# Kernel optimization log

Hardware: AMD Instinct MI355X
Metric: run time of the kernel (lower is better)

The kernel has to match this reference:

```python
import jax, jax.numpy as jnp
import numpy as np

N = 10000          # nodes
E = 160000         # edges (avg degree 16)
F = 240            # invariant features_dim
H_INV, D_INV = 4, 60    # invariant heads / head dim
H_EV, D_EV = 3, 80      # equivariant heads (= len(degrees)) / head dim
RBF = 32
DEGREES = [1, 2, 3]
REPEATS = np.array([2 * l + 1 for l in DEGREES])   # [3,5,7]
EV_DIM = int(REPEATS.sum())                        # 15
OFFS = np.concatenate([[0], np.cumsum(REPEATS)])   # [0,3,8,15]


def _kaiming_uniform(key, shape, fan_in):
    # torch kaiming_uniform_ with a=sqrt(5): bound = 1/sqrt(fan_in)
    b = 1.0 / np.sqrt(fan_in)
    return jax.random.uniform(key, shape, minval=-b, maxval=b, dtype=jnp.float32)


def setup_inputs() -> dict:
    key = jax.random.key(0)
    ks = jax.random.split(key, 16)
    return {
        "inv_features": jax.random.normal(ks[0], (N, F), dtype=jnp.float32),
        "ev_features": jax.random.normal(ks[1], (N, EV_DIM), dtype=jnp.float32),
        "rbf": jax.random.uniform(ks[2], (E, RBF), dtype=jnp.float32),
        "sh_vectors": jax.random.normal(ks[3], (E, EV_DIM), dtype=jnp.float32),
        "cutoffs": jax.random.uniform(ks[4], (E, 1), dtype=jnp.float32),
        "W_q_inv": _kaiming_uniform(ks[5], (H_INV, D_INV, D_INV), D_INV),
        "W_k_inv": _kaiming_uniform(ks[6], (H_INV, D_INV, D_INV), D_INV),
        "W_v_inv": _kaiming_uniform(ks[7], (H_INV, D_INV, D_INV), D_INV),
        "W_q_ev": _kaiming_uniform(ks[8], (H_EV, D_EV, D_EV), D_EV),
        "W_k_ev": _kaiming_uniform(ks[9], (H_EV, D_EV, D_EV), D_EV),
        "W_filt_inv": _kaiming_uniform(ks[10], (RBF + len(DEGREES), F), RBF + len(DEGREES)),
        "b_filt_inv": jnp.zeros((F,), dtype=jnp.float32),
        "W_filt_ev": _kaiming_uniform(ks[11], (RBF + len(DEGREES), F), RBF + len(DEGREES)),
        "b_filt_ev": jnp.zeros((F,), dtype=jnp.float32),
        "senders": jax.random.randint(ks[12], (E,), 0, N, dtype=jnp.int32),
        "receivers": jax.random.randint(ks[13], (E,), 0, N, dtype=jnp.int32),
    }


def reference(inv_features, ev_features, rbf, sh_vectors, cutoffs,
              W_q_inv, W_k_inv, W_v_inv, W_q_ev, W_k_ev,
              W_filt_inv, b_filt_inv, W_filt_ev, b_filt_ev,
              senders, receivers):
    n = inv_features.shape[0]
    # edge-wise equivariant differences [E, 15]
    ev_diff = ev_features[senders] - ev_features[receivers]
    # per-degree SO3 invariants: sum over m components of each degree -> [E, 3]
    invs = jnp.stack([(ev_diff[:, OFFS[i]:OFFS[i + 1]] ** 2).sum(-1)
                      for i in range(len(DEGREES))], axis=-1)
    f_in = jnp.concatenate([rbf, invs], axis=-1)           # [E, RBF+3]
    fw_inv = (f_in @ W_filt_inv + b_filt_inv).reshape(-1, H_INV, D_INV)
    fw_ev = (f_in @ W_filt_ev + b_filt_ev).reshape(-1, H_EV, D_EV)

    xi = inv_features.reshape(-1, H_INV, D_INV)
    xe = inv_features.reshape(-1, H_EV, D_EV)
    q_inv = jnp.einsum('hij,nhi->nhj', W_q_inv, xi)[receivers]
    k_inv = jnp.einsum('hij,nhi->nhj', W_k_inv, xi)[senders]
    v_inv = jnp.einsum('hij,nhi->nhj', W_v_inv, xi)[senders]
    q_ev = jnp.einsum('hij,nhi->nhj', W_q_ev, xe)[receivers]
    k_ev = jnp.einsum('hij,nhi->nhj', W_k_ev, xe)[senders]

    alpha_inv = (q_inv * (k_inv * fw_inv)).sum(-1, keepdims=True) / np.sqrt(D_INV)  # [E,H,1]
    alpha_ev = (q_ev * (k_ev * fw_ev)).sum(-1) / np.sqrt(D_EV)                      # [E,3]

    scaled_inv = cutoffs[:, None] * alpha_inv * v_inv       # [E,H,D]
    d_inv = jax.ops.segment_sum(scaled_inv, receivers, num_segments=n).reshape(n, -1)

    alpha_ev_r = jnp.repeat(alpha_ev, REPEATS, axis=-1, total_repeat_length=EV_DIM)  # [E,15]
    scaled_ev = cutoffs * alpha_ev_r * sh_vectors
    d_ev = jax.ops.segment_sum(scaled_ev, receivers, num_segments=n)
    return d_inv, d_ev
```

## Files before the change

### kernel.cpp

```cpp
#include <hip/hip_runtime.h>

#define PNPB 32

__global__ __launch_bounds__(512) void proj_kernel(
    const float* __restrict__ x,
    const float* __restrict__ Wq, const float* __restrict__ Wk,
    const float* __restrict__ Wv,
    const float* __restrict__ Wqe, const float* __restrict__ Wke,
    float* __restrict__ q_inv, float* __restrict__ k_inv,
    float* __restrict__ v_inv,
    float* __restrict__ q_ev, float* __restrict__ k_ev, int N)
{
    __shared__ float xs[PNPB * 240];
    const int base_node = blockIdx.x * PNPB;
    for (int idx = threadIdx.x; idx < PNPB * 240; idx += 512) {
        int g = base_node * 240 + idx;
        xs[idx] = (g < N * 240) ? x[g] : 0.f;
    }
    __syncthreads();

    const int slot = threadIdx.x & 63;
    const int wg   = threadIdx.x >> 6;
    if (slot >= 60) return;

    const int hi  = slot / 15;
    const int jdi = slot * 4 - hi * 60;
    const int he  = slot / 20;
    const int jde = slot * 4 - he * 80;
    const int nl0 = wg * 4;

    float4 aq[4], ak[4], av[4], aqe[4], ake[4];
    #pragma unroll
    for (int n = 0; n < 4; ++n) {
        aq[n] = make_float4(0.f,0.f,0.f,0.f); ak[n] = aq[n]; av[n] = aq[n];
        aqe[n] = aq[n]; ake[n] = aq[n];
    }
    {
        const float* wq = Wq + hi * 3600 + jdi;
        const float* wk = Wk + hi * 3600 + jdi;
        const float* wv = Wv + hi * 3600 + jdi;
        const float* xb = &xs[nl0 * 240 + hi * 60];
        #pragma unroll 2
        for (int i = 0; i < 60; ++i) {
            float xv0 = xb[i], xv1 = xb[240 + i], xv2 = xb[480 + i], xv3 = xb[720 + i];
            float4 w;
            w = *(const float4*)&wq[i * 60];
            aq[0].x += xv0*w.x; aq[0].y += xv0*w.y; aq[0].z += xv0*w.z; aq[0].w += xv0*w.w;
            aq[1].x += xv1*w.x; aq[1].y += xv1*w.y; aq[1].z += xv1*w.z; aq[1].w += xv1*w.w;
            aq[2].x += xv2*w.x; aq[2].y += xv2*w.y; aq[2].z += xv2*w.z; aq[2].w += xv2*w.w;
            aq[3].x += xv3*w.x; aq[3].y += xv3*w.y; aq[3].z += xv3*w.z; aq[3].w += xv3*w.w;
            w = *(const float4*)&wk[i * 60];
            ak[0].x += xv0*w.x; ak[0].y += xv0*w.y; ak[0].z += xv0*w.z; ak[0].w += xv0*w.w;
            ak[1].x += xv1*w.x; ak[1].y += xv1*w.y; ak[1].z += xv1*w.z; ak[1].w += xv1*w.w;
            ak[2].x += xv2*w.x; ak[2].y += xv2*w.y; ak[2].z += xv2*w.z; ak[2].w += xv2*w.w;
            ak[3].x += xv3*w.x; ak[3].y += xv3*w.y; ak[3].z += xv3*w.z; ak[3].w += xv3*w.w;
            w = *(const float4*)&wv[i * 60];
            av[0].x += xv0*w.x; av[0].y += xv0*w.y; av[0].z += xv0*w.z; av[0].w += xv0*w.w;
            av[1].x += xv1*w.x; av[1].y += xv1*w.y; av[1].z += xv1*w.z; av[1].w += xv1*w.w;
            av[2].x += xv2*w.x; av[2].y += xv2*w.y; av[2].z += xv2*w.z; av[2].w += xv2*w.w;
            av[3].x += xv3*w.x; av[3].y += xv3*w.y; av[3].z += xv3*w.z; av[3].w += xv3*w.w;
        }
    }
    {
        const float* wq = Wqe + he * 6400 + jde;
        const float* wk = Wke + he * 6400 + jde;
        const float* xb = &xs[nl0 * 240 + he * 80];
        #pragma unroll 2
        for (int i = 0; i < 80; ++i) {
            float xv0 = xb[i], xv1 = xb[240 + i], xv2 = xb[480 + i], xv3 = xb[720 + i];
            float4 w;
            w = *(const float4*)&wq[i * 80];
            aqe[0].x += xv0*w.x; aqe[0].y += xv0*w.y; aqe[0].z += xv0*w.z; aqe[0].w += xv0*w.w;
            aqe[1].x += xv1*w.x; aqe[1].y += xv1*w.y; aqe[1].z += xv1*w.z; aqe[1].w += xv1*w.w;
            aqe[2].x += xv2*w.x; aqe[2].y += xv2*w.y; aqe[2].z += xv2*w.z; aqe[2].w += xv2*w.w;
            aqe[3].x += xv3*w.x; aqe[3].y += xv3*w.y; aqe[3].z += xv3*w.z; aqe[3].w += xv3*w.w;
            w = *(const float4*)&wk[i * 80];
            ake[0].x += xv0*w.x; ake[0].y += xv0*w.y; ake[0].z += xv0*w.z; ake[0].w += xv0*w.w;
            ake[1].x += xv1*w.x; ake[1].y += xv1*w.y; ake[1].z += xv1*w.z; ake[1].w += xv1*w.w;
            ake[2].x += xv2*w.x; ake[2].y += xv2*w.y; ake[2].z += xv2*w.z; ake[2].w += xv2*w.w;
            ake[3].x += xv3*w.x; ake[3].y += xv3*w.y; ake[3].z += xv3*w.z; ake[3].w += xv3*w.w;
        }
    }
    #pragma unroll
    for (int n = 0; n < 4; ++n) {
        const int node = base_node + nl0 + n;
        if (node >= N) break;
        const int ob = node * 240 + slot * 4;
        *(float4*)&q_inv[ob] = aq[n];
        *(float4*)&k_inv[ob] = ak[n];
        *(float4*)&v_inv[ob] = av[n];
        *(float4*)&q_ev[ob]  = aqe[n];
        *(float4*)&k_ev[ob]  = ake[n];
    }
}

__global__ __launch_bounds__(256) void hist_kernel(
    const int* __restrict__ rcv, int* __restrict__ counts, int E)
{
    int e = blockIdx.x * 256 + threadIdx.x;
    if (e < E) atomicAdd(&counts[rcv[e]], 1);
}

__global__ __launch_bounds__(1024) void scan_kernel(
    const int* __restrict__ counts, int* __restrict__ rowstart,
    int* __restrict__ cursor, int N)
{
    __shared__ int wsum[16];
    __shared__ int carry_s;
    if (threadIdx.x == 0) carry_s = 0;
    __syncthreads();
    const int lane = threadIdx.x & 63;
    const int w    = threadIdx.x >> 6;
    for (int base = 0; base < N; base += 1024) {
        const int i = base + threadIdx.x;
        int v = (i < N) ? counts[i] : 0;
        int x = v;
        #pragma unroll
        for (int off = 1; off < 64; off <<= 1) {
            int t = __shfl_up(x, off);
            if (lane >= off) x += t;
        }
        if (lane == 63) wsum[w] = x;
        __syncthreads();
        if (w == 0) {
            int s = (lane < 16) ? wsum[lane] : 0;
            #pragma unroll
            for (int off = 1; off < 16; off <<= 1) {
                int t = __shfl_up(s, off);
                if (lane >= off) s += t;
            }
            if (lane < 16) wsum[lane] = s;
        }
        __syncthreads();
        const int woff = (w == 0) ? 0 : wsum[w - 1];
        const int ex = carry_s + woff + x - v;
        if (i < N) { rowstart[i] = ex; cursor[i] = ex; }
        __syncthreads();
        if (threadIdx.x == 1023) carry_s += wsum[15];
    }
    __syncthreads();
    if (threadIdx.x == 0) rowstart[N] = carry_s;
}

__global__ __launch_bounds__(256) void scatter_kernel(
    const int* __restrict__ rcv, int* __restrict__ cursor,
    int* __restrict__ csr, int E)
{
    int e = blockIdx.x * 256 + threadIdx.x;
    if (e < E) {
        int pos = atomicAdd(&cursor[rcv[e]], 1);
        csr[pos] = e;
    }
}

__global__ __launch_bounds__(256) void inv3_kernel(
    const float* __restrict__ ev_f, const int* __restrict__ snd,
    const int* __restrict__ rcv, float* __restrict__ inv3, int E)
{
    int e = blockIdx.x * 256 + threadIdx.x;
    if (e >= E) return;
    const float* es = ev_f + (size_t)snd[e] * 15;
    const float* er = ev_f + (size_t)rcv[e] * 15;
    float i0 = 0.f, i1 = 0.f, i2 = 0.f;
    #pragma unroll
    for (int q = 0; q < 3; ++q)  { float d = es[q] - er[q]; i0 = fmaf(d, d, i0); }
    #pragma unroll
    for (int q = 3; q < 8; ++q)  { float d = es[q] - er[q]; i1 = fmaf(d, d, i1); }
    #pragma unroll
    for (int q = 8; q < 15; ++q) { float d = es[q] - er[q]; i2 = fmaf(d, d, i2); }
    *(float4*)(inv3 + (size_t)e * 4) = make_float4(i0, i1, i2, 0.f);
}

__global__ __launch_bounds__(256, 1) void alpha_inv_kernel(
    const float* __restrict__ rbf, const float* __restrict__ inv3,
    const float* __restrict__ cut,
    const float* __restrict__ Wfi, const float* __restrict__ bfi,
    const int* __restrict__ snd, const int* __restrict__ rcv,
    const int* __restrict__ csr,
    const float* __restrict__ q_inv, const float* __restrict__ k_inv,
    float* __restrict__ alpha, int E)
{
    __shared__ float fs[4][64 * 36];
    __shared__ int   ss[4][64], sr[4][64];

    const int lane = threadIdx.x & 63;
    const int wid  = threadIdx.x >> 6;
    const int h = lane >> 4;
    const int m = lane & 15;
    const bool act = (m < 15);
    const int j0 = h * 60 + (act ? m * 4 : 0);

    float4 w[35];
    #pragma unroll
    for (int k = 0; k < 35; ++k)
        w[k] = *(const float4*)(Wfi + k * 240 + j0);
    const float4 b4 = *(const float4*)(bfi + j0);
    const float s60 = 0.12909944487358056f;

    const int tbase = (blockIdx.x * 4 + wid) * 64;
    {
        int i = tbase + lane;
        if (i >= E) i = E - 1;
        const int e = csr[i];
        float* frow = &fs[wid][lane * 36];
        const float4* rb = (const float4*)(rbf + (size_t)e * 32);
        #pragma unroll
        for (int k4 = 0; k4 < 8; ++k4)
            *(float4*)&frow[k4 * 4] = rb[k4];
        const float4 v3 = *(const float4*)(inv3 + (size_t)e * 4);
        frow[32] = v3.x; frow[33] = v3.y; frow[34] = v3.z;
        frow[35] = cut[e];
        ss[wid][lane] = snd[e];
        sr[wid][lane] = rcv[e];
    }
    __syncthreads();

    #pragma unroll 2
    for (int t = 0; t < 64; ++t) {
        const int gi = tbase + t;
        if (gi >= E) break;
        const int s = ss[wid][t];
        const int r = sr[wid][t];
        const float* frow = &fs[wid][t * 36];

        float4 fw = b4;
        #pragma unroll
        for (int k4 = 0; k4 < 8; ++k4) {
            const float4 f4 = *(const float4*)&frow[k4 * 4];
            const float4 w0 = w[k4*4+0], w1 = w[k4*4+1], w2 = w[k4*4+2], w3 = w[k4*4+3];
            fw.x = fmaf(f4.x, w0.x, fw.x); fw.y = fmaf(f4.x, w0.y, fw.y);
            fw.z = fmaf(f4.x, w0.z, fw.z); fw.w = fmaf(f4.x, w0.w, fw.w);
            fw.x = fmaf(f4.y, w1.x, fw.x); fw.y = fmaf(f4.y, w1.y, fw.y);
            fw.z = fmaf(f4.y, w1.z, fw.z); fw.w = fmaf(f4.y, w1.w, fw.w);
            fw.x = fmaf(f4.z, w2.x, fw.x); fw.y = fmaf(f4.z, w2.y, fw.y);
            fw.z = fmaf(f4.z, w2.z, fw.z); fw.w = fmaf(f4.z, w2.w, fw.w);
            fw.x = fmaf(f4.w, w3.x, fw.x); fw.y = fmaf(f4.w, w3.y, fw.y);
            fw.z = fmaf(f4.w, w3.z, fw.z); fw.w = fmaf(f4.w, w3.w, fw.w);
        }
        {
            const float fa = frow[32], fb = frow[33], fc = frow[34];
            const float4 wa = w[32], wb = w[33], wc = w[34];
            fw.x = fmaf(fa, wa.x, fw.x); fw.y = fmaf(fa, wa.y, fw.y);
            fw.z = fmaf(fa, wa.z, fw.z); fw.w = fmaf(fa, wa.w, fw.w);
            fw.x = fmaf(fb, wb.x, fw.x); fw.y = fmaf(fb, wb.y, fw.y);
            fw.z = fmaf(fb, wb.z, fw.z); fw.w = fmaf(fb, wb.w, fw.w);
            fw.x = fmaf(fc, wc.x, fw.x); fw.y = fmaf(fc, wc.y, fw.y);
            fw.z = fmaf(fc, wc.z, fw.z); fw.w = fmaf(fc, wc.w, fw.w);
        }
        const float cc = frow[35];

        const float4 q  = *(const float4*)(q_inv + (size_t)r * 240 + j0);
        const float4 kk = *(const float4*)(k_inv + (size_t)s * 240 + j0);
        float d = act ? (q.x*kk.x*fw.x + q.y*kk.y*fw.y
                       + q.z*kk.z*fw.z + q.w*kk.w*fw.w) : 0.f;
        #pragma unroll
        for (int off = 1; off < 16; off <<= 1) d += __shfl_xor(d, off, 16);
        if (m == 0)    alpha[(size_t)gi * 8 + h] = d * s60 * cc;
        if (lane == 0) alpha[(size_t)gi * 8 + 7] = __int_as_float(s);
    }
}

__global__ __launch_bounds__(256, 1) void alpha_ev_kernel(
    const float* __restrict__ rbf, const float* __restrict__ inv3,
    const float* __restrict__ cut,
    const float* __restrict__ Wfe, const float* __restrict__ bfe,
    const int* __restrict__ snd, const int* __restrict__ rcv,
    const int* __restrict__ csr,
    const float* __restrict__ q_ev, const float* __restrict__ k_ev,
    float* __restrict__ alpha, int E)
{
    __shared__ float fs[4][64 * 36];
    __shared__ int   ss[4][64], sr[4][64];

    const int lane = threadIdx.x & 63;
    const int wid  = threadIdx.x >> 6;
    const bool act = (lane < 60);
    const int h = act ? (lane / 20) : 0;
    const int m = act ? (lane % 20) : 0;
    const int j0 = 80 * h + 4 * m;

    float4 w[35];
    #pragma unroll
    for (int k = 0; k < 35; ++k)
        w[k] = *(const float4*)(Wfe + k * 240 + j0);
    const float4 b4 = *(const float4*)(bfe + j0);
    const float s80 = 0.11180339887498948f;

    const int tbase = (blockIdx.x * 4 + wid) * 64;
    {
        int i = tbase + lane;
        if (i >= E) i = E - 1;
        const int e = csr[i];
        float* frow = &fs[wid][lane * 36];
        const float4* rb = (const float4*)(rbf + (size_t)e * 32);
        #pragma unroll
        for (int k4 = 0; k4 < 8; ++k4)
            *(float4*)&frow[k4 * 4] = rb[k4];
        const float4 v3 = *(const float4*)(inv3 + (size_t)e * 4);
        frow[32] = v3.x; frow[33] = v3.y; frow[34] = v3.z;
        frow[35] = cut[e];
        ss[wid][lane] = snd[e];
        sr[wid][lane] = rcv[e];
    }
    __syncthreads();

    #pragma unroll 2
    for (int t = 0; t < 64; ++t) {
        const int gi = tbase + t;
        if (gi >= E) break;
        const int s = ss[wid][t];
        const int r = sr[wid][t];
        const float* frow = &fs[wid][t * 36];

        float4 fw = b4;
        #pragma unroll
        for (int k4 = 0; k4 < 8; ++k4) {
            const float4 f4 = *(const float4*)&frow[k4 * 4];
            const float4 w0 = w[k4*4+0], w1 = w[k4*4+1], w2 = w[k4*4+2], w3 = w[k4*4+3];
            fw.x = fmaf(f4.x, w0.x, fw.x); fw.y = fmaf(f4.x, w0.y, fw.y);
            fw.z = fmaf(f4.x, w0.z, fw.z); fw.w = fmaf(f4.x, w0.w, fw.w);
            fw.x = fmaf(f4.y, w1.x, fw.x); fw.y = fmaf(f4.y, w1.y, fw.y);
            fw.z = fmaf(f4.y, w1.z, fw.z); fw.w = fmaf(f4.y, w1.w, fw.w);
            fw.x = fmaf(f4.z, w2.x, fw.x); fw.y = fmaf(f4.z, w2.y, fw.y);
            fw.z = fmaf(f4.z, w2.z, fw.z); fw.w = fmaf(f4.z, w2.w, fw.w);
            fw.x = fmaf(f4.w, w3.x, fw.x); fw.y = fmaf(f4.w, w3.y, fw.y);
            fw.z = fmaf(f4.w, w3.z, fw.z); fw.w = fmaf(f4.w, w3.w, fw.w);
        }
        {
            const float fa = frow[32], fb = frow[33], fc = frow[34];
            const float4 wa = w[32], wb = w[33], wc = w[34];
            fw.x = fmaf(fa, wa.x, fw.x); fw.y = fmaf(fa, wa.y, fw.y);
            fw.z = fmaf(fa, wa.z, fw.z); fw.w = fmaf(fa, wa.w, fw.w);
            fw.x = fmaf(fb, wb.x, fw.x); fw.y = fmaf(fb, wb.y, fw.y);
            fw.z = fmaf(fb, wb.z, fw.z); fw.w = fmaf(fb, wb.w, fw.w);
            fw.x = fmaf(fc, wc.x, fw.x); fw.y = fmaf(fc, wc.y, fw.y);
            fw.z = fmaf(fc, wc.z, fw.z); fw.w = fmaf(fc, wc.w, fw.w);
        }
        const float cc = frow[35];

        const float4 q  = *(const float4*)(q_ev + (size_t)r * 240 + j0);
        const float4 kk = *(const float4*)(k_ev + (size_t)s * 240 + j0);
        float d = act ? (q.x*kk.x*fw.x + q.y*kk.y*fw.y
                       + q.z*kk.z*fw.z + q.w*kk.w*fw.w) : 0.f;

        float tt;
        tt = __shfl(d, (lane + 10) & 63); if (m < 10) d += tt;
        tt = __shfl(d, (lane + 5) & 63);  if (m < 5)  d += tt;
        const int gb = h * 20;
        const float t1 = __shfl(d, gb + 1);
        const float t2 = __shfl(d, gb + 2);
        const float t3 = __shfl(d, gb + 3);
        const float t4 = __shfl(d, gb + 4);
        if (act && m == 0)
            alpha[(size_t)gi * 8 + 4 + h] = (d + t1 + t2 + t3 + t4) * s80 * cc;
    }
}

__global__ __launch_bounds__(256) void gather_kernel(
    const int* __restrict__ rowstart, const int* __restrict__ csr,
    const float* __restrict__ alpha,
    const float* __restrict__ v_inv, const float* __restrict__ sh,
    float* __restrict__ dinv, float* __restrict__ dev)
{
    const int r = blockIdx.x;
    const int c = threadIdx.x;
    const int beg = rowstart[r], end = rowstart[r + 1];

    __shared__ float sal[64][8];
    __shared__ int   sed[64];

    float acc = 0.f;
    for (int chunk = beg; chunk < end; chunk += 64) {
        const int len = min(64, end - chunk);
        __syncthreads();
        if (c < len) {
            const float4* ap = (const float4*)(alpha + (size_t)(chunk + c) * 8);
            const float4 a0 = ap[0], a1 = ap[1];
            *(float4*)&sal[c][0] = a0;
            *(float4*)&sal[c][4] = a1;
            sed[c] = csr[chunk + c];
        }
        __syncthreads();
        if (c < 240) {
            const int h = c / 60;
            #pragma unroll 4
            for (int i = 0; i < len; ++i) {
                const int s = __float_as_int(sal[i][7]);
                acc += sal[i][h] * v_inv[(size_t)s * 240 + c];
            }
        } else if (c < 255) {
            const int i0 = c - 240;
            const int h = (i0 < 3) ? 4 : ((i0 < 8) ? 5 : 6);
            for (int i = 0; i < len; ++i)
                acc += sal[i][h] * sh[(size_t)sed[i] * 15 + i0];
        }
    }
    if (c < 240) dinv[(size_t)r * 240 + c] = acc;
    else if (c < 255) dev[(size_t)r * 15 + (c - 240)] = acc;
}

extern "C" void kernel_launch(void* const* d_in, const int* in_sizes, int n_in,
                              void* d_out, int out_size, void* d_ws, size_t ws_size,
                              hipStream_t stream) {
    const float* inv_f = (const float*)d_in[0];
    const float* ev_f  = (const float*)d_in[1];
    const float* rbf   = (const float*)d_in[2];
    const float* sh    = (const float*)d_in[3];
    const float* cut   = (const float*)d_in[4];
    const float* Wq    = (const float*)d_in[5];
    const float* Wk    = (const float*)d_in[6];
    const float* Wv    = (const float*)d_in[7];
    const float* Wqe   = (const float*)d_in[8];
    const float* Wke   = (const float*)d_in[9];
    const float* Wfi   = (const float*)d_in[10];
    const float* bfi   = (const float*)d_in[11];
    const float* Wfe   = (const float*)d_in[12];
    const float* bfe   = (const float*)d_in[13];
    const int*   snd   = (const int*)d_in[14];
    const int*   rcv   = (const int*)d_in[15];

    const int N = in_sizes[0] / 240;
    const int E = in_sizes[14];

    float* out  = (float*)d_out;
    float* dinv = out;
    float* dev  = out + (size_t)N * 240;

    float* ws = (float*)d_ws;
    const size_t Nf = (size_t)N * 240;
    float* q_inv = ws + 0 * Nf;
    float* k_inv = ws + 1 * Nf;
    float* v_inv = ws + 2 * Nf;
    float* q_ev  = ws + 3 * Nf;
    float* k_ev  = ws + 4 * Nf;
    float* alpha = ws + 5 * Nf;
    float* inv3  = alpha + (size_t)E * 8;
    int*   ibase    = (int*)(inv3 + (size_t)E * 4);
    int*   counts   = ibase;
    int*   rowstart = ibase + N;
    int*   cursor   = ibase + 2 * N + 1;
    int*   csr      = ibase + 3 * N + 1;

    hipMemsetAsync(counts, 0, (size_t)N * sizeof(int), stream);

    const int eb = (E + 255) / 256;
    hist_kernel<<<eb, 256, 0, stream>>>(rcv, counts, E);
    scan_kernel<<<1, 1024, 0, stream>>>(counts, rowstart, cursor, N);
    scatter_kernel<<<eb, 256, 0, stream>>>(rcv, cursor, csr, E);

    proj_kernel<<<(N + PNPB - 1) / PNPB, 512, 0, stream>>>(
        inv_f, Wq, Wk, Wv, Wqe, Wke, q_inv, k_inv, v_inv, q_ev, k_ev, N);

    inv3_kernel<<<eb, 256, 0, stream>>>(ev_f, snd, rcv, inv3, E);

    const int ab = (E + 255) / 256;
    alpha_inv_kernel<<<ab, 256, 0, stream>>>(
        rbf, inv3, cut, Wfi, bfi, snd, rcv, csr, q_inv, k_inv, alpha, E);
    alpha_ev_kernel<<<ab, 256, 0, stream>>>(
        rbf, inv3, cut, Wfe, bfe, snd, rcv, csr, q_ev, k_ev, alpha, E);

    gather_kernel<<<N, 256, 0, stream>>>(
        rowstart, csr, alpha, v_inv, sh, dinv, dev);
}
```

Before: 386.5 us.

## Merge inv/ev alpha kernels into one 2D-grid launch with smaller tiles

The two per-edge attention-score kernels become one kernel, with blockIdx.y choosing the invariant or equivariant branch. The per-wave edge tile shrinks from 64 to 32, which doubles the block count and reduces shared memory per block. Launch bounds rise from 1 to 4 blocks per SM, aiming for more concurrent waves to hide the gather latency on q/k rows. The cost is that the 35 weight float4s per lane are loaded twice as often, and register pressure must now fit the higher occupancy target.

```diff
diff --git a/kernel.cpp b/kernel.cpp
--- a/kernel.cpp
+++ b/kernel.cpp
@@ -1,6 +1,7 @@
 #include <hip/hip_runtime.h>
 
 #define PNPB 32
+#define TILE 32
 
 __global__ __launch_bounds__(512) void proj_kernel(
     const float* __restrict__ x,
@@ -171,34 +172,49 @@
     *(float4*)(inv3 + (size_t)e * 4) = make_float4(i0, i1, i2, 0.f);
 }
 
-__global__ __launch_bounds__(256, 1) void alpha_inv_kernel(
+__global__ __launch_bounds__(256, 4) void alpha_fused_kernel(
     const float* __restrict__ rbf, const float* __restrict__ inv3,
     const float* __restrict__ cut,
     const float* __restrict__ Wfi, const float* __restrict__ bfi,
+    const float* __restrict__ Wfe, const float* __restrict__ bfe,
     const int* __restrict__ snd, const int* __restrict__ rcv,
     const int* __restrict__ csr,
     const float* __restrict__ q_inv, const float* __restrict__ k_inv,
+    const float* __restrict__ q_ev,  const float* __restrict__ k_ev,
     float* __restrict__ alpha, int E)
 {
-    __shared__ float fs[4][64 * 36];
-    __shared__ int   ss[4][64], sr[4][64];
+    __shared__ float fs[4][TILE * 36];
+    __shared__ int   ss[4][TILE], sr[4][TILE];
 
     const int lane = threadIdx.x & 63;
     const int wid  = threadIdx.x >> 6;
-    const int h = lane >> 4;
-    const int m = lane & 15;
-    const bool act = (m < 15);
-    const int j0 = h * 60 + (act ? m * 4 : 0);
+    const int part = blockIdx.y;
+
+    int h, m, j0; bool act;
+    if (part == 0) {
+        h = lane >> 4; m = lane & 15; act = (m < 15);
+        j0 = h * 60 + (act ? m * 4 : 0);
+    } else {
+        act = (lane < 60);
+        h = act ? (lane / 20) : 0;
+        m = act ? (lane % 20) : 0;
+        j0 = 80 * h + 4 * m;
+    }
+
+    const float* Wf = part ? Wfe : Wfi;
+    const float* bf = part ? bfe : bfi;
+    const float* qbase = part ? q_ev : q_inv;
+    const float* kbase = part ? k_ev : k_inv;
+    const float scale = part ? 0.11180339887498948f : 0.12909944487358056f;
 
     float4 w[35];
     #pragma unroll
     for (int k = 0; k < 35; ++k)
-        w[k] = *(const float4*)(Wfi + k * 240 + j0);
-    const float4 b4 = *(const float4*)(bfi + j0);
-    const float s60 = 0.12909944487358056f;
-
-    const int tbase = (blockIdx.x * 4 + wid) * 64;
-    {
+        w[k] = *(const float4*)(Wf + k * 240 + j0);
+    const float4 b4 = *(const float4*)(bf + j0);
+
+    const int tbase = (blockIdx.x * 4 + wid) * TILE;
+    if (lane < TILE) {
         int i = tbase + lane;
         if (i >= E) i = E - 1;
         const int e = csr[i];
@@ -216,7 +232,7 @@
     __syncthreads();
 
     #pragma unroll 2
-    for (int t = 0; t < 64; ++t) {
+    for (int t = 0; t < TILE; ++t) {
         const int gi = tbase + t;
         if (gi >= E) break;
         const int s = ss[wid][t];
@@ -249,110 +265,28 @@
         }
         const float cc = frow[35];
 
-        const float4 q  = *(const float4*)(q_inv + (size_t)r * 240 + j0);
-        const float4 kk = *(const float4*)(k_inv + (size_t)s * 240 + j0);
+        const float4 q  = *(const float4*)(qbase + (size_t)r * 240 + j0);
+        const float4 kk = *(const float4*)(kbase + (size_t)s * 240 + j0);
         float d = act ? (q.x*kk.x*fw.x + q.y*kk.y*fw.y
                        + q.z*kk.z*fw.z + q.w*kk.w*fw.w) : 0.f;
-        #pragma unroll
-        for (int off = 1; off < 16; off <<= 1) d += __shfl_xor(d, off, 16);
-        if (m == 0)    alpha[(size_t)gi * 8 + h] = d * s60 * cc;
-        if (lane == 0) alpha[(size_t)gi * 8 + 7] = __int_as_float(s);
-    }
-}
-
-__global__ __launch_bounds__(256, 1) void alpha_ev_kernel(
-    const float* __restrict__ rbf, const float* __restrict__ inv3,
-    const float* __restrict__ cut,
-    const float* __restrict__ Wfe, const float* __restrict__ bfe,
-    const int* __restrict__ snd, const int* __restrict__ rcv,
-    const int* __restrict__ csr,
-    const float* __restrict__ q_ev, const float* __restrict__ k_ev,
-    float* __restrict__ alpha, int E)
-{
-    __shared__ float fs[4][64 * 36];
-    __shared__ int   ss[4][64], sr[4][64];
-
-    const int lane = threadIdx.x & 63;
-    const int wid  = threadIdx.x >> 6;
-    const bool act = (lane < 60);
-    const int h = act ? (lane / 20) : 0;
-    const int m = act ? (lane % 20) : 0;
-    const int j0 = 80 * h + 4 * m;
-
-    float4 w[35];
-    #pragma unroll
-    for (int k = 0; k < 35; ++k)
-        w[k] = *(const float4*)(Wfe + k * 240 + j0);
-    const float4 b4 = *(const float4*)(bfe + j0);
-    const float s80 = 0.11180339887498948f;
-
-    const int tbase = (blockIdx.x * 4 + wid) * 64;
-    {
-        int i = tbase + lane;
-        if (i >= E) i = E - 1;
-        const int e = csr[i];
-        float* frow = &fs[wid][lane * 36];
-        const float4* rb = (const float4*)(rbf + (size_t)e * 32);
-        #pragma unroll
-        for (int k4 = 0; k4 < 8; ++k4)
-            *(float4*)&frow[k4 * 4] = rb[k4];
-        const float4 v3 = *(const float4*)(inv3 + (size_t)e * 4);
-        frow[32] = v3.x; frow[33] = v3.y; frow[34] = v3.z;
-        frow[35] = cut[e];
-        ss[wid][lane] = snd[e];
-        sr[wid][lane] = rcv[e];
-    }
-    __syncthreads();
-
-    #pragma unroll 2
-    for (int t = 0; t < 64; ++t) {
-        const int gi = tbase + t;
-        if (gi >= E) break;
-        const int s = ss[wid][t];
-        const int r = sr[wid][t];
-        const float* frow = &fs[wid][t * 36];
-
-        float4 fw = b4;
-        #pragma unroll
-        for (int k4 = 0; k4 < 8; ++k4) {
-            const float4 f4 = *(const float4*)&frow[k4 * 4];
-            const float4 w0 = w[k4*4+0], w1 = w[k4*4+1], w2 = w[k4*4+2], w3 = w[k4*4+3];
-            fw.x = fmaf(f4.x, w0.x, fw.x); fw.y = fmaf(f4.x, w0.y, fw.y);
-            fw.z = fmaf(f4.x, w0.z, fw.z); fw.w = fmaf(f4.x, w0.w, fw.w);
-            fw.x = fmaf(f4.y, w1.x, fw.x); fw.y = fmaf(f4.y, w1.y, fw.y);
-            fw.z = fmaf(f4.y, w1.z, fw.z); fw.w = fmaf(f4.y, w1.w, fw.w);
-            fw.x = fmaf(f4.z, w2.x, fw.x); fw.y = fmaf(f4.z, w2.y, fw.y);
-            fw.z = fmaf(f4.z, w2.z, fw.z); fw.w = fmaf(f4.z, w2.w, fw.w);
-            fw.x = fmaf(f4.w, w3.x, fw.x); fw.y = fmaf(f4.w, w3.y, fw.y);
-            fw.z = fmaf(f4.w, w3.z, fw.z); fw.w = fmaf(f4.w, w3.w, fw.w);
-        }
-        {
-            const float fa = frow[32], fb = frow[33], fc = frow[34];
-            const float4 wa = w[32], wb = w[33], wc = w[34];
-            fw.x = fmaf(fa, wa.x, fw.x); fw.y = fmaf(fa, wa.y, fw.y);
-            fw.z = fmaf(fa, wa.z, fw.z); fw.w = fmaf(fa, wa.w, fw.w);
-            fw.x = fmaf(fb, wb.x, fw.x); fw.y = fmaf(fb, wb.y, fw.y);
-            fw.z = fmaf(fb, wb.z, fw.z); fw.w = fmaf(fb, wb.w, fw.w);
-            fw.x = fmaf(fc, wc.x, fw.x); fw.y = fmaf(fc, wc.y, fw.y);
-            fw.z = fmaf(fc, wc.z, fw.z); fw.w = fmaf(fc, wc.w, fw.w);
-        }
-        const float cc = frow[35];
-
-        const float4 q  = *(const float4*)(q_ev + (size_t)r * 240 + j0);
-        const float4 kk = *(const float4*)(k_ev + (size_t)s * 240 + j0);
-        float d = act ? (q.x*kk.x*fw.x + q.y*kk.y*fw.y
-                       + q.z*kk.z*fw.z + q.w*kk.w*fw.w) : 0.f;
-
-        float tt;
-        tt = __shfl(d, (lane + 10) & 63); if (m < 10) d += tt;
-        tt = __shfl(d, (lane + 5) & 63);  if (m < 5)  d += tt;
-        const int gb = h * 20;
-        const float t1 = __shfl(d, gb + 1);
-        const float t2 = __shfl(d, gb + 2);
-        const float t3 = __shfl(d, gb + 3);
-        const float t4 = __shfl(d, gb + 4);
-        if (act && m == 0)
-            alpha[(size_t)gi * 8 + 4 + h] = (d + t1 + t2 + t3 + t4) * s80 * cc;
+
+        if (part == 0) {
+            #pragma unroll
+            for (int off = 1; off < 16; off <<= 1) d += __shfl_xor(d, off, 16);
+            if (m == 0)    alpha[(size_t)gi * 8 + h] = d * scale * cc;
+            if (lane == 0) alpha[(size_t)gi * 8 + 7] = __int_as_float(s);
+        } else {
+            float tt;
+            tt = __shfl(d, (lane + 10) & 63); if (m < 10) d += tt;
+            tt = __shfl(d, (lane + 5) & 63);  if (m < 5)  d += tt;
+            const int gb = h * 20;
+            const float t1 = __shfl(d, gb + 1);
+            const float t2 = __shfl(d, gb + 2);
+            const float t3 = __shfl(d, gb + 3);
+            const float t4 = __shfl(d, gb + 4);
+            if (act && m == 0)
+                alpha[(size_t)gi * 8 + 4 + h] = (d + t1 + t2 + t3 + t4) * scale * cc;
+        }
     }
 }
 
@@ -453,11 +387,10 @@
 
     inv3_kernel<<<eb, 256, 0, stream>>>(ev_f, snd, rcv, inv3, E);
 
-    const int ab = (E + 255) / 256;
-    alpha_inv_kernel<<<ab, 256, 0, stream>>>(
-        rbf, inv3, cut, Wfi, bfi, snd, rcv, csr, q_inv, k_inv, alpha, E);
-    alpha_ev_kernel<<<ab, 256, 0, stream>>>(
-        rbf, inv3, cut, Wfe, bfe, snd, rcv, csr, q_ev, k_ev, alpha, E);
+    const int ab = (E + 4 * TILE - 1) / (4 * TILE);
+    alpha_fused_kernel<<<dim3(ab, 2), 256, 0, stream>>>(
+        rbf, inv3, cut, Wfi, bfi, Wfe, bfe, snd, rcv, csr,
+        q_inv, k_inv, q_ev, k_ev, alpha, E);
 
     gather_kernel<<<N, 256, 0, stream>>>(
         rowstart, csr, alpha, v_inv, sh, dinv, dev);
```

Result: slower. 949.5 us (+145.7%).
